# Optimization experiments

Hardware: AMD Instinct MI355X
Metric: run time of the kernel (lower is better)

## Reference

```python
import jax, jax.numpy as jnp
import numpy as np
import math


def _rotary_cos_sin(seq_len, head_dim, base=10000.0):
    # Matches SEDD's Rotary: cos/sin of shape [1, s, 3, 1, d], with the
    # v-slice (index 2 of the 'three' axis) set to identity (cos=1, sin=0).
    inv_freq = 1.0 / (base ** (np.arange(0, head_dim, 2, dtype=np.float32) / head_dim))
    t = np.arange(seq_len, dtype=np.float32)
    freqs = np.einsum('i,j->ij', t, inv_freq)          # [s, d/2]
    emb = np.concatenate([freqs, freqs], axis=-1)       # [s, d]
    cos = np.tile(np.cos(emb)[None, :, None, None, :], (1, 1, 3, 1, 1))
    sin = np.tile(np.sin(emb)[None, :, None, None, :], (1, 1, 3, 1, 1))
    cos[:, :, 2] = 1.0
    sin[:, :, 2] = 0.0
    return jnp.asarray(cos, dtype=jnp.float32), jnp.asarray(sin, dtype=jnp.float32)


def _rotate_half(x):
    x1, x2 = jnp.split(x, 2, axis=-1)
    return jnp.concatenate([-x2, x1], axis=-1)


def setup_inputs() -> dict:
    key = jax.random.key(0)
    B, S, H, D = 2, 2048, 12, 64
    k1, k2 = jax.random.split(key)
    qkv = jax.random.normal(k1, (B, S, 3, H, D), dtype=jnp.float32)
    cos, sin = _rotary_cos_sin(S, D)
    seqlens = jax.random.randint(k2, (B,), 1024, S + 1).astype(jnp.int32)
    return {"qkv": qkv, "cos": cos, "sin": sin, "seqlens": seqlens}


def reference(qkv, cos, sin, seqlens):
    B, S, _, H, D = qkv.shape
    # rotary applied to all of qkv; v slice of cos/sin is identity
    qkv = qkv * cos + _rotate_half(qkv) * sin
    # split and reshape to (b, h, s, d)
    q = jnp.transpose(qkv[:, :, 0], (0, 2, 1, 3))
    k = jnp.transpose(qkv[:, :, 1], (0, 2, 1, 3))
    v = jnp.transpose(qkv[:, :, 2], (0, 2, 1, 3))
    # padding mask from ragged seqlens
    valid = jnp.arange(S, dtype=jnp.int32)[None, :] < seqlens[:, None]   # [b, s]
    mask = valid[:, :, None] & valid[:, None, :]                          # [b, i, j]
    attn_logits = jnp.einsum('bhid,bhjd->bhij', q, k) / math.sqrt(D)
    attn_logits = jnp.where(mask[:, None, :, :], attn_logits, -1e10)
    attn = jax.nn.softmax(attn_logits, axis=-1)
    x = jnp.einsum('bhij,bhjd->bhid', attn, v)
    return x, attn_logits
```

## Files before the change

### kernel.cpp

```cpp
#include <hip/hip_runtime.h>
#include <hip/hip_bf16.h>
#include <math.h>

#define SLEN 2048
#define NH   12
#define NB   2
#define DH   64
#define IT   64
#define JT   64
#define NWAVE 4
#define LDP  72

typedef __bf16 bfx8 __attribute__((ext_vector_type(8)));
typedef float  f32x4 __attribute__((ext_vector_type(4)));

__global__ __launch_bounds__(256)
void ddit_prep(const float* __restrict__ qkv,
               const float* __restrict__ cosb,
               const float* __restrict__ sinb,
               __bf16* __restrict__ Qr, __bf16* __restrict__ Kr,
               __bf16* __restrict__ Vt)
{
    __shared__ __align__(16) __bf16 Vlds[64 * LDP];
    const int tid = threadIdx.x;
    const int nS  = SLEN / 64;
    const int s0  = (blockIdx.x % nS) * 64;
    const int bh  = blockIdx.x / nS;
    const int h   = bh % NH;
    const int b   = bh / NH;
    const int r   = tid >> 2;
    const int d0  = (tid & 3) * 16;
    const int s   = s0 + r;

#pragma unroll
    for (int t = 0; t < 2; ++t) {
        const float* src = qkv + (((size_t)((size_t)b * SLEN + s) * 3 + t) * NH + h) * DH;
        const float* cs  = cosb + ((size_t)s * 3 + t) * DH;
        const float* sn  = sinb + ((size_t)s * 3 + t) * DH;
        union { __bf16 hv[16]; uint4 u4[2]; } pk;
#pragma unroll
        for (int dd = 0; dd < 16; dd += 4) {
            const int d = d0 + dd;
            float4 f  = *(const float4*)(src + d);
            float4 g  = *(const float4*)(src + (d ^ 32));
            float4 c4 = *(const float4*)(cs + d);
            float4 s4 = *(const float4*)(sn + d);
            const float sg = (d < 32) ? -1.f : 1.f;
            pk.hv[dd + 0] = (__bf16)(f.x * c4.x + sg * g.x * s4.x);
            pk.hv[dd + 1] = (__bf16)(f.y * c4.y + sg * g.y * s4.y);
            pk.hv[dd + 2] = (__bf16)(f.z * c4.z + sg * g.z * s4.z);
            pk.hv[dd + 3] = (__bf16)(f.w * c4.w + sg * g.w * s4.w);
        }
        __bf16* dst = (t == 0 ? Qr : Kr) + ((size_t)bh * SLEN + s) * DH + d0;
        *(uint4*)(dst + 0) = pk.u4[0];
        *(uint4*)(dst + 8) = pk.u4[1];
    }

    {
        const float* src = qkv + (((size_t)((size_t)b * SLEN + s) * 3 + 2) * NH + h) * DH;
#pragma unroll
        for (int dd = 0; dd < 16; dd += 4) {
            float4 f = *(const float4*)(src + d0 + dd);
            union { __bf16 hv[4]; uint2 u; } pk;
            pk.hv[0] = (__bf16)f.x; pk.hv[1] = (__bf16)f.y;
            pk.hv[2] = (__bf16)f.z; pk.hv[3] = (__bf16)f.w;
            *(uint2*)(Vlds + r * LDP + d0 + dd) = pk.u;
        }
    }
    __syncthreads();
    {
        const int dv   = tid >> 2;
        const int soff = (tid & 3) * 16;
        union { __bf16 hv[16]; uint4 u4[2]; } pk;
#pragma unroll
        for (int j = 0; j < 16; ++j)
            pk.hv[j] = Vlds[(soff + j) * LDP + dv];
        __bf16* dst = Vt + ((size_t)bh * DH + dv) * SLEN + s0 + soff;
        *(uint4*)(dst + 0) = pk.u4[0];
        *(uint4*)(dst + 8) = pk.u4[1];
    }
}

__global__ __launch_bounds__(256)
void ddit_attn(const __bf16* __restrict__ Qr,
               const __bf16* __restrict__ Kr,
               const __bf16* __restrict__ Vt,
               const int*   __restrict__ seqlens,
               float* __restrict__ out_x,
               float* __restrict__ out_logits)
{
    __shared__ __align__(16) __bf16 Pbuf[NWAVE * 16 * LDP];

    const int tid  = threadIdx.x;
    const int wave = tid >> 6;
    const int lane = tid & 63;
    const int qd   = lane >> 4;
    const int m    = lane & 15;

    const int nIt   = SLEN / IT;
    const int gridN = NB * NH * nIt;
    const int bid   = blockIdx.x;
    const int nid   = (bid & 7) * (gridN >> 3) + (bid >> 3);
    const int it    = nid % nIt;
    const int bh    = nid / nIt;
    const int b     = bh / NH;
    const int i0    = it * IT;
    const int len   = seqlens[b];

    const __bf16* Qb = Qr + (size_t)bh * SLEN * DH;
    const __bf16* Kb = Kr + (size_t)bh * SLEN * DH;
    const __bf16* Vb = Vt + (size_t)bh * DH * SLEN;
    float* logits_base = out_logits + (size_t)bh * SLEN * SLEN;

    bfx8 qfrag[2];
#pragma unroll
    for (int c = 0; c < 2; ++c)
        qfrag[c] = *(const bfx8*)(Qb + (size_t)(i0 + wave * 16 + m) * DH + c * 32 + qd * 8);

    float mrun[4], lrun[4];
    f32x4 acc[4];
#pragma unroll
    for (int r = 0; r < 4; ++r) { mrun[r] = -3.0e38f; lrun[r] = 0.f; }
#pragma unroll
    for (int c = 0; c < 4; ++c) acc[c] = (f32x4){0.f, 0.f, 0.f, 0.f};

    const int irow_base = i0 + wave * 16 + qd * 4;
    __bf16* myP = Pbuf + wave * 16 * LDP;

    for (int j0 = 0; j0 < SLEN; j0 += JT) {
        bfx8 kf[4][2];
#pragma unroll
        for (int t4 = 0; t4 < 4; ++t4)
#pragma unroll
            for (int c = 0; c < 2; ++c)
                kf[t4][c] = *(const bfx8*)(Kb + (size_t)(j0 + t4 * 16 + m) * DH + c * 32 + qd * 8);

        f32x4 sacc[4];
#pragma unroll
        for (int t4 = 0; t4 < 4; ++t4) {
            sacc[t4] = (f32x4){0.f, 0.f, 0.f, 0.f};
#pragma unroll
            for (int c = 0; c < 2; ++c)
                sacc[t4] = __builtin_amdgcn_mfma_f32_16x16x32_bf16(qfrag[c], kf[t4][c], sacc[t4], 0, 0, 0);
        }

        bfx8 vf[2][4];
#pragma unroll
        for (int kc = 0; kc < 2; ++kc)
#pragma unroll
            for (int c = 0; c < 4; ++c)
                vf[kc][c] = *(const bfx8*)(Vb + (size_t)(c * 16 + m) * SLEN + j0 + kc * 32 + qd * 8);

        float ls[4][4];
#pragma unroll
        for (int t4 = 0; t4 < 4; ++t4) {
            const int jG = j0 + t4 * 16 + m;
            const bool vj = jG < len;
#pragma unroll
            for (int r = 0; r < 4; ++r) {
                const int iG = irow_base + r;
                const bool ok = vj && (iG < len);
                const float lv = ok ? sacc[t4][r] * 0.125f : -1.0e10f;
                ls[t4][r] = lv;
                logits_base[(size_t)iG * SLEN + jG] = lv;
            }
        }

#pragma unroll
        for (int r = 0; r < 4; ++r) {
            float mt = fmaxf(fmaxf(ls[0][r], ls[1][r]), fmaxf(ls[2][r], ls[3][r]));
#pragma unroll
            for (int off = 1; off < 16; off <<= 1)
                mt = fmaxf(mt, __shfl_xor(mt, off));
            const float mn = fmaxf(mrun[r], mt);
            const float al = __expf(mrun[r] - mn);
            float p[4], ps = 0.f;
#pragma unroll
            for (int t4 = 0; t4 < 4; ++t4) { p[t4] = __expf(ls[t4][r] - mn); ps += p[t4]; }
#pragma unroll
            for (int off = 1; off < 16; off <<= 1)
                ps += __shfl_xor(ps, off);
            lrun[r] = lrun[r] * al + ps;
            mrun[r] = mn;
#pragma unroll
            for (int c = 0; c < 4; ++c) acc[c][r] *= al;
#pragma unroll
            for (int t4 = 0; t4 < 4; ++t4)
                myP[(qd * 4 + r) * LDP + t4 * 16 + m] = (__bf16)p[t4];
        }

#pragma unroll
        for (int kc = 0; kc < 2; ++kc) {
            bfx8 pf = *(const bfx8*)&myP[m * LDP + kc * 32 + qd * 8];
#pragma unroll
            for (int c = 0; c < 4; ++c)
                acc[c] = __builtin_amdgcn_mfma_f32_16x16x32_bf16(pf, vf[kc][c], acc[c], 0, 0, 0);
        }
    }

#pragma unroll
    for (int r = 0; r < 4; ++r) {
        const int iG = irow_base + r;
        const float inv = 1.f / lrun[r];
#pragma unroll
        for (int c = 0; c < 4; ++c)
            out_x[((size_t)bh * SLEN + iG) * DH + c * 16 + m] = acc[c][r] * inv;
    }
}

extern "C" void kernel_launch(void* const* d_in, const int* in_sizes, int n_in,
                              void* d_out, int out_size, void* d_ws, size_t ws_size,
                              hipStream_t stream) {
    const float* qkv     = (const float*)d_in[0];
    const float* cosb    = (const float*)d_in[1];
    const float* sinb    = (const float*)d_in[2];
    const int*   seqlens = (const int*)d_in[3];
    float* out_x      = (float*)d_out;
    float* out_logits = out_x + (size_t)NB * NH * SLEN * DH;

    const size_t perT = (size_t)NB * NH * SLEN * DH;
    __bf16* Qr = (__bf16*)d_ws;
    __bf16* Kr = Qr + perT;
    __bf16* Vt = Kr + perT;

    dim3 block(256);
    ddit_prep<<<dim3(NB * NH * (SLEN / 64)), block, 0, stream>>>(qkv, cosb, sinb, Qr, Kr, Vt);
    ddit_attn<<<dim3(NB * NH * (SLEN / IT)), block, 0, stream>>>(Qr, Kr, Vt, seqlens, out_x, out_logits);
}
```

Baseline: 581.1 us.

## Skip masked tiles, transpose score MFMA for vector logit stores, prefetch K

Query tiles entirely past seqlen skip QK and softmax: they write the constant -1e10 logits and compute the uniform average of V directly. Fully valid query tiles stop the QK loop at the padded seqlen and fill the remaining logits with the constant. The score MFMA operands are swapped so each lane holds four consecutive j values, which allows 16-byte nontemporal logit stores and a simpler row-wise softmax reduction. K fragments for the next tile are prefetched. This adds shuffles to broadcast the per-row rescale and normaliser, and more code paths.

```diff
diff --git a/kernel.cpp b/kernel.cpp
--- a/kernel.cpp
+++ b/kernel.cpp
@@ -110,38 +110,81 @@
     const __bf16* Qb = Qr + (size_t)bh * SLEN * DH;
     const __bf16* Kb = Kr + (size_t)bh * SLEN * DH;
     const __bf16* Vb = Vt + (size_t)bh * DH * SLEN;
-    float* logits_base = out_logits + (size_t)bh * SLEN * SLEN;
+
+    const int iG_lane = i0 + wave * 16 + m;
+    float* lrow = out_logits + (size_t)bh * SLEN * SLEN + (size_t)iG_lane * SLEN;
+    __bf16* myP = Pbuf + wave * 16 * LDP;
+
+    f32x4 acc[4];
+#pragma unroll
+    for (int c = 0; c < 4; ++c) acc[c] = (f32x4){0.f, 0.f, 0.f, 0.f};
+    const f32x4 NEG4 = (f32x4){-1.0e10f, -1.0e10f, -1.0e10f, -1.0e10f};
+
+    if (i0 >= len) {
+        union { __bf16 h[4]; uint2 u; } ones;
+#pragma unroll
+        for (int r = 0; r < 4; ++r) ones.h[r] = (__bf16)1.0f;
+#pragma unroll
+        for (int t4 = 0; t4 < 4; ++t4)
+            *(uint2*)(myP + m * LDP + t4 * 16 + qd * 4) = ones.u;
+        bfx8 pf1[2];
+#pragma unroll
+        for (int kc = 0; kc < 2; ++kc)
+            pf1[kc] = *(const bfx8*)&myP[m * LDP + kc * 32 + qd * 8];
+
+        for (int j0 = 0; j0 < SLEN; j0 += JT) {
+            bfx8 vf[2][4];
+#pragma unroll
+            for (int kc = 0; kc < 2; ++kc)
+#pragma unroll
+                for (int c = 0; c < 4; ++c)
+                    vf[kc][c] = *(const bfx8*)(Vb + (size_t)(c * 16 + m) * SLEN + j0 + kc * 32 + qd * 8);
+#pragma unroll
+            for (int t4 = 0; t4 < 4; ++t4)
+                __builtin_nontemporal_store(NEG4, (f32x4*)(lrow + j0 + t4 * 16 + qd * 4));
+#pragma unroll
+            for (int kc = 0; kc < 2; ++kc)
+#pragma unroll
+                for (int c = 0; c < 4; ++c)
+                    acc[c] = __builtin_amdgcn_mfma_f32_16x16x32_bf16(pf1[kc], vf[kc][c], acc[c], 0, 0, 0);
+        }
+        const float inv = 1.0f / (float)SLEN;
+#pragma unroll
+        for (int r = 0; r < 4; ++r) {
+            const int iG = i0 + wave * 16 + qd * 4 + r;
+#pragma unroll
+            for (int c = 0; c < 4; ++c)
+                out_x[((size_t)bh * SLEN + iG) * DH + c * 16 + m] = acc[c][r] * inv;
+        }
+        return;
+    }
+
+    const bool full_i = (i0 + IT <= len);
+    const int  jlim   = full_i ? ((len + JT - 1) & ~(JT - 1)) : SLEN;
+    const bool vi     = iG_lane < len;
 
     bfx8 qfrag[2];
 #pragma unroll
     for (int c = 0; c < 2; ++c)
-        qfrag[c] = *(const bfx8*)(Qb + (size_t)(i0 + wave * 16 + m) * DH + c * 32 + qd * 8);
-
-    float mrun[4], lrun[4];
-    f32x4 acc[4];
-#pragma unroll
-    for (int r = 0; r < 4; ++r) { mrun[r] = -3.0e38f; lrun[r] = 0.f; }
-#pragma unroll
-    for (int c = 0; c < 4; ++c) acc[c] = (f32x4){0.f, 0.f, 0.f, 0.f};
-
-    const int irow_base = i0 + wave * 16 + qd * 4;
-    __bf16* myP = Pbuf + wave * 16 * LDP;
-
-    for (int j0 = 0; j0 < SLEN; j0 += JT) {
-        bfx8 kf[4][2];
-#pragma unroll
-        for (int t4 = 0; t4 < 4; ++t4)
-#pragma unroll
-            for (int c = 0; c < 2; ++c)
-                kf[t4][c] = *(const bfx8*)(Kb + (size_t)(j0 + t4 * 16 + m) * DH + c * 32 + qd * 8);
-
+        qfrag[c] = *(const bfx8*)(Qb + (size_t)iG_lane * DH + c * 32 + qd * 8);
+
+    bfx8 kf[4][2];
+#pragma unroll
+    for (int t4 = 0; t4 < 4; ++t4)
+#pragma unroll
+        for (int c = 0; c < 2; ++c)
+            kf[t4][c] = *(const bfx8*)(Kb + (size_t)(t4 * 16 + m) * DH + c * 32 + qd * 8);
+
+    float mrun = -3.0e38f, lrun = 0.f;
+
+    for (int j0 = 0; j0 < jlim; j0 += JT) {
         f32x4 sacc[4];
 #pragma unroll
         for (int t4 = 0; t4 < 4; ++t4) {
             sacc[t4] = (f32x4){0.f, 0.f, 0.f, 0.f};
 #pragma unroll
             for (int c = 0; c < 2; ++c)
-                sacc[t4] = __builtin_amdgcn_mfma_f32_16x16x32_bf16(qfrag[c], kf[t4][c], sacc[t4], 0, 0, 0);
+                sacc[t4] = __builtin_amdgcn_mfma_f32_16x16x32_bf16(kf[t4][c], qfrag[c], sacc[t4], 0, 0, 0);
         }
 
         bfx8 vf[2][4];
@@ -151,57 +194,83 @@
             for (int c = 0; c < 4; ++c)
                 vf[kc][c] = *(const bfx8*)(Vb + (size_t)(c * 16 + m) * SLEN + j0 + kc * 32 + qd * 8);
 
+        {
+            const int jn = (j0 + JT < SLEN) ? (j0 + JT) : 0;
+#pragma unroll
+            for (int t4 = 0; t4 < 4; ++t4)
+#pragma unroll
+                for (int c = 0; c < 2; ++c)
+                    kf[t4][c] = *(const bfx8*)(Kb + (size_t)(jn + t4 * 16 + m) * DH + c * 32 + qd * 8);
+        }
+
         float ls[4][4];
 #pragma unroll
         for (int t4 = 0; t4 < 4; ++t4) {
-            const int jG = j0 + t4 * 16 + m;
-            const bool vj = jG < len;
+            f32x4 lv;
 #pragma unroll
             for (int r = 0; r < 4; ++r) {
-                const int iG = irow_base + r;
-                const bool ok = vj && (iG < len);
-                const float lv = ok ? sacc[t4][r] * 0.125f : -1.0e10f;
-                ls[t4][r] = lv;
-                logits_base[(size_t)iG * SLEN + jG] = lv;
+                const int jG = j0 + t4 * 16 + qd * 4 + r;
+                const bool ok = vi && (jG < len);
+                lv[r] = ok ? sacc[t4][r] * 0.125f : -1.0e10f;
+                ls[t4][r] = lv[r];
             }
-        }
+            __builtin_nontemporal_store(lv, (f32x4*)(lrow + j0 + t4 * 16 + qd * 4));
+        }
+
+        float smax = ls[0][0];
+#pragma unroll
+        for (int t4 = 0; t4 < 4; ++t4)
+#pragma unroll
+            for (int r = 0; r < 4; ++r) smax = fmaxf(smax, ls[t4][r]);
+        smax = fmaxf(smax, __shfl_xor(smax, 16));
+        smax = fmaxf(smax, __shfl_xor(smax, 32));
+        const float mn = fmaxf(mrun, smax);
+        const float al = __expf(mrun - mn);
+        float psum = 0.f;
+        union { __bf16 h[4]; uint2 u; } pk[4];
+#pragma unroll
+        for (int t4 = 0; t4 < 4; ++t4)
+#pragma unroll
+            for (int r = 0; r < 4; ++r) {
+                const float p = __expf(ls[t4][r] - mn);
+                psum += p;
+                pk[t4].h[r] = (__bf16)p;
+            }
+        psum += __shfl_xor(psum, 16);
+        psum += __shfl_xor(psum, 32);
+        lrun = lrun * al + psum;
+        mrun = mn;
+
+#pragma unroll
+        for (int t4 = 0; t4 < 4; ++t4)
+            *(uint2*)(myP + m * LDP + t4 * 16 + qd * 4) = pk[t4].u;
 
 #pragma unroll
         for (int r = 0; r < 4; ++r) {
-            float mt = fmaxf(fmaxf(ls[0][r], ls[1][r]), fmaxf(ls[2][r], ls[3][r]));
-#pragma unroll
-            for (int off = 1; off < 16; off <<= 1)
-                mt = fmaxf(mt, __shfl_xor(mt, off));
-            const float mn = fmaxf(mrun[r], mt);
-            const float al = __expf(mrun[r] - mn);
-            float p[4], ps = 0.f;
-#pragma unroll
-            for (int t4 = 0; t4 < 4; ++t4) { p[t4] = __expf(ls[t4][r] - mn); ps += p[t4]; }
-#pragma unroll
-            for (int off = 1; off < 16; off <<= 1)
-                ps += __shfl_xor(ps, off);
-            lrun[r] = lrun[r] * al + ps;
-            mrun[r] = mn;
-#pragma unroll
-            for (int c = 0; c < 4; ++c) acc[c][r] *= al;
-#pragma unroll
-            for (int t4 = 0; t4 < 4; ++t4)
-                myP[(qd * 4 + r) * LDP + t4 * 16 + m] = (__bf16)p[t4];
+            const float alr = __shfl(al, qd * 4 + r);
+#pragma unroll
+            for (int c = 0; c < 4; ++c) acc[c][r] *= alr;
         }
 
 #pragma unroll
         for (int kc = 0; kc < 2; ++kc) {
-            bfx8 pf = *(const bfx8*)&myP[m * LDP + kc * 32 + qd * 8];
+            const bfx8 pf = *(const bfx8*)&myP[m * LDP + kc * 32 + qd * 8];
 #pragma unroll
             for (int c = 0; c < 4; ++c)
                 acc[c] = __builtin_amdgcn_mfma_f32_16x16x32_bf16(pf, vf[kc][c], acc[c], 0, 0, 0);
         }
     }
 
+    for (int j0 = jlim; j0 < SLEN; j0 += JT)
+#pragma unroll
+        for (int t4 = 0; t4 < 4; ++t4)
+            __builtin_nontemporal_store(NEG4, (f32x4*)(lrow + j0 + t4 * 16 + qd * 4));
+
 #pragma unroll
     for (int r = 0; r < 4; ++r) {
-        const int iG = irow_base + r;
-        const float inv = 1.f / lrun[r];
+        const float lr  = __shfl(lrun, qd * 4 + r);
+        const float inv = 1.0f / lr;
+        const int   iG  = i0 + wave * 16 + qd * 4 + r;
 #pragma unroll
         for (int c = 0; c < 4; ++c)
             out_x[((size_t)bh * SLEN + iG) * DH + c * 16 + m] = acc[c][r] * inv;
```

New measurement: 566.9 us. 1.02x faster.
